# Optimization experiments

Hardware: AMD Instinct MI355X
Metric: run time of the kernel (lower is better)

The kernel has to match this reference:

```python
import jax, jax.numpy as jnp
import numpy as np

B, S, D, H, F, M, DC = 2, 1024, 1024, 16, 4096, 2048, 256
HD = D // H

def rmsnorm(x, w, eps=1e-6):
    return x * jax.lax.rsqrt(jnp.mean(x * x, axis=-1, keepdims=True) + eps) * w

def setup_inputs() -> dict:
    key = jax.random.key(0)
    ks = jax.random.split(key, 16)
    def w(i, shape):
        return jax.random.normal(ks[i], shape, jnp.float32) * (1.0 / np.sqrt(shape[0]))
    # real RoPE tables
    inv = 1.0 / (10000.0 ** (jnp.arange(0, HD, 2, dtype=jnp.float32) / HD))
    freqs = jnp.outer(jnp.arange(S, dtype=jnp.float32), inv)
    emb = jnp.concatenate([freqs, freqs], axis=-1)  # [S, HD]
    return {
        "hidden_states": jax.random.normal(ks[0], (B, S, D), jnp.float32),
        "mem_keys": jnp.zeros((B, M, DC), jnp.float32),
        "mem_values": jnp.zeros((B, M, D), jnp.float32),
        "cos": jnp.cos(emb), "sin": jnp.sin(emb),
        "norm1_w": jnp.ones((D,), jnp.float32),
        "norm2_w": jnp.ones((D,), jnp.float32),
        "norm_mem_w": jnp.ones((D,), jnp.float32),
        "Wq": w(1, (D, D)), "Wk": w(2, (D, D)), "Wv": w(3, (D, D)), "Wo": w(4, (D, D)),
        "W_content": w(5, (D, D)), "W_comp": w(6, (D, DC)), "W_strength": w(7, (D, 1)),
        "W_query": w(8, (D, DC)),
        "W_gate": w(9, (2 * D, D)), "W_proj": w(10, (D, D)),
        "W1": w(11, (D, F)), "W3": w(12, (D, F)), "W2": w(13, (F, D)),
        "position": 0,
    }

def reference(hidden_states, mem_keys, mem_values, cos, sin,
              norm1_w, norm2_w, norm_mem_w,
              Wq, Wk, Wv, Wo,
              W_content, W_comp, W_strength, W_query,
              W_gate, W_proj, W1, W3, W2, position):
    b, s, d = hidden_states.shape
    h = hidden_states
    # 1) causal self-attention with RoPE
    n = rmsnorm(h, norm1_w)
    def heads(x):
        return x.reshape(b, s, H, HD).transpose(0, 2, 1, 3)  # [b,h,s,hd]
    q, k, v = heads(n @ Wq), heads(n @ Wk), heads(n @ Wv)
    def rot(x):
        x1, x2 = jnp.split(x, 2, axis=-1)
        return jnp.concatenate([-x2, x1], axis=-1)
    c, si = cos[None, None], sin[None, None]
    q = q * c + rot(q) * si
    k = k * c + rot(k) * si
    scores = jnp.einsum('bhqd,bhkd->bhqk', q, k) / np.sqrt(HD)
    causal = jnp.tril(jnp.ones((s, s), bool))
    scores = jnp.where(causal, scores, jnp.float32(-1e30))
    attn = jax.nn.softmax(scores, axis=-1)
    attn_out = jnp.einsum('bhqk,bhkd->bhqd', attn, v).transpose(0, 2, 1, 3).reshape(b, s, d) @ Wo
    h = h + attn_out
    # 2) memory snapshot write: the original per-token python loop writes each token
    #    to consecutive circular-buffer slots; with M >= s the slots are unique, so
    #    the loop vectorizes into a single scatter.
    content = h @ W_content                     # [b,s,d]
    compressed = h @ W_comp                     # [b,s,DC]
    strength = jax.nn.sigmoid(h @ W_strength)   # [b,s,1]
    idx = (position + jnp.arange(s)) % mem_keys.shape[1]
    old_k = mem_keys[:, idx]
    old_v = mem_values[:, idx]
    new_keys = mem_keys.at[:, idx].set(strength * compressed + (1.0 - strength) * old_k)
    new_values = mem_values.at[:, idx].set(strength * content + (1.0 - strength) * old_v)
    # 3) memory retrieval (attention over slots)
    normed = rmsnorm(h, norm_mem_w)
    qm = normed @ W_query                       # [b,s,DC]
    mscores = jnp.einsum('bsd,bmd->bsm', qm, new_keys) / np.sqrt(DC)
    mattn = jax.nn.softmax(mscores, axis=-1)
    retrieved = jnp.einsum('bsm,bmd->bsd', mattn, new_values)
    # 4) gated memory integration
    gate = jax.nn.sigmoid(jnp.concatenate([h, retrieved], axis=-1) @ W_gate)
    h = h + gate * (retrieved @ W_proj)
    # 5) SwiGLU FFN
    n2 = rmsnorm(h, norm2_w)
    h = h + (jax.nn.silu(n2 @ W1) * (n2 @ W3)) @ W2
    return (h, new_keys, new_values)
```

## Files before the change

### kernel.cpp

```cpp
#include <hip/hip_runtime.h>
#include <hip/hip_bf16.h>
#include <math.h>

typedef __bf16 bf16;
typedef __attribute__((ext_vector_type(8))) __bf16 bf16x8;
typedef __attribute__((ext_vector_type(4))) __bf16 bf16x4;
typedef __attribute__((ext_vector_type(4))) float f32x4;

#define B_ 2
#define S_ 1024
#define D_ 1024
#define H_ 16
#define HD_ 64
#define F_ 4096
#define M_ 2048
#define DC_ 256
#define NTOK (B_*S_)

__device__ __forceinline__ void gload16(const void* g, void* l) {
    __builtin_amdgcn_global_load_lds(
        (__attribute__((address_space(1))) void*)(void*)(g),
        (__attribute__((address_space(3))) void*)(l), 16, 0, 0);
}

template<int N> __device__ __forceinline__ void wait_vm() {
    if constexpr (N == 0)      asm volatile("s_waitcnt vmcnt(0)" ::: "memory");
    else if constexpr (N == 2) asm volatile("s_waitcnt vmcnt(2)" ::: "memory");
    else if constexpr (N == 4) asm volatile("s_waitcnt vmcnt(4)" ::: "memory");
    else if constexpr (N == 6) asm volatile("s_waitcnt vmcnt(6)" ::: "memory");
    else                       asm volatile("s_waitcnt vmcnt(8)" ::: "memory");
}
__device__ __forceinline__ void wait_lgkm0() {
    asm volatile("s_waitcnt lgkmcnt(0)" ::: "memory");
}
__device__ __forceinline__ float sigm(float x) { return 1.f / (1.f + expf(-x)); }

template<int BM, int BN, bool OUTBF, int EPI>
__global__ __launch_bounds__(256) void mgemm(
    const bf16* __restrict__ A, const bf16* __restrict__ Bt,
    const float* __restrict__ resid, void* __restrict__ Cout,
    int K, int lda, int ldb, int ldc,
    long long sA, long long sB, long long sC,
    const void* __restrict__ aux1, const void* __restrict__ aux2)
{
    constexpr int WN   = (BM == 128) ? 2 : 4;
    constexpr int WCOL = BN / WN;
    constexpr int FN   = WCOL / 16;
    constexpr int LA = BM * 64, LB = BN * 64;
    constexpr int LPS = BM / 32 + BN / 32;
    __shared__ bf16 lds[2 * (LA + LB)];
    const int z = blockIdx.z;
    A  += (size_t)z * sA;
    Bt += (size_t)z * sB;
    const int gx = gridDim.x;
    const int nwg = gx * gridDim.y;
    const int flat = blockIdx.y * gx + blockIdx.x;
    const int q8 = nwg >> 3, r8 = nwg & 7;
    const int xcd = flat & 7, lid = flat >> 3;
    const int swz = (xcd < r8 ? xcd * (q8 + 1) : r8 * (q8 + 1) + (xcd - r8) * q8) + lid;
    const int band = swz / (8 * gx);
    const int rem  = swz % (8 * gx);
    const int row0 = (band * 8 + (rem & 7)) * BM;
    const int col0 = (rem >> 3) * BN;
    const int tid = threadIdx.x, wid = tid >> 6, lane = tid & 63;
    const int wr = wid / WN, wc = wid % WN;
    const int srow = lane >> 3;
    const int ssub = (lane & 7) ^ (srow & 7);

    f32x4 acc[4][FN];
    #pragma unroll
    for (int m = 0; m < 4; ++m)
        #pragma unroll
        for (int n = 0; n < FN; ++n) acc[m][n] = (f32x4){0.f, 0.f, 0.f, 0.f};

    auto STAGE = [&](int buf, int k0) {
        bf16* Ab = lds + buf * (LA + LB);
        bf16* Bb = Ab + LA;
        #pragma unroll
        for (int i = 0; i < BM / 32; ++i) {
            int c = wid * (BM / 32) + i;
            gload16(A + (size_t)(row0 + c * 8 + srow) * lda + k0 + ssub * 8, Ab + c * 512);
        }
        #pragma unroll
        for (int i = 0; i < BN / 32; ++i) {
            int c = wid * (BN / 32) + i;
            gload16(Bt + (size_t)(col0 + c * 8 + srow) * ldb + k0 + ssub * 8, Bb + c * 512);
        }
    };

    const int nt = K >> 6;
    STAGE(0, 0);
    if (nt > 1) STAGE(1, 64);
    for (int t = 0; t < nt; ++t) {
        if (t < nt - 1) wait_vm<LPS>();
        else            wait_vm<0>();
        __builtin_amdgcn_sched_barrier(0);
        __builtin_amdgcn_s_barrier();
        __builtin_amdgcn_sched_barrier(0);
        const bf16* Ab = lds + (t & 1) * (LA + LB);
        const bf16* Bb = Ab + LA;
        const int ar = wr * 64 + (lane & 15);
        const int br = wc * WCOL + (lane & 15);
        #pragma unroll
        for (int ksel = 0; ksel < 2; ++ksel) {
            const int ps = ((ksel << 2) + (lane >> 4)) ^ (lane & 7);
            bf16x8 af[4], bfr[FN];
            #pragma unroll
            for (int m = 0; m < 4; ++m)
                af[m] = *(const bf16x8*)(Ab + (ar + m * 16) * 64 + ps * 8);
            #pragma unroll
            for (int n = 0; n < FN; ++n)
                bfr[n] = *(const bf16x8*)(Bb + (br + n * 16) * 64 + ps * 8);
            #pragma unroll
            for (int m = 0; m < 4; ++m)
                #pragma unroll
                for (int n = 0; n < FN; ++n)
                    acc[m][n] = __builtin_amdgcn_mfma_f32_16x16x32_bf16(af[m], bfr[n], acc[m][n], 0, 0, 0);
        }
        wait_lgkm0();
        __builtin_amdgcn_sched_barrier(0);
        __builtin_amdgcn_s_barrier();
        __builtin_amdgcn_sched_barrier(0);
        if (t + 2 < nt) STAGE(t & 1, (t + 2) << 6);
    }
    const int crow = row0 + wr * 64 + ((lane >> 4) << 2);
    const int ccol = col0 + wc * WCOL + (lane & 15);
    #pragma unroll
    for (int m = 0; m < 4; ++m)
        #pragma unroll
        for (int n = 0; n < FN; ++n)
            #pragma unroll
            for (int r = 0; r < 4; ++r) {
                const int rr = crow + m * 16 + r, cc = ccol + n * 16;
                size_t idx = (size_t)rr * ldc + cc;
                float v = acc[m][n][r];
                if (EPI == 2) {
                    float g = sigm(((const float*)aux1)[idx]);
                    v = ((const float*)aux2)[idx] + g * v;
                    ((float*)Cout)[idx] = v;
                } else {
                    if (resid) v += resid[idx];
                    if (OUTBF) ((bf16*)Cout)[(size_t)z * sC + idx] = (bf16)v;
                    else       ((float*)Cout)[(size_t)z * sC + idx] = v;
                    if (EPI == 1)
                        ((bf16*)aux1)[(size_t)rr * 2048 + cc] = (bf16)v;
                }
            }
}

__global__ __launch_bounds__(256) void mgemm13(
    const bf16* __restrict__ A, const bf16* __restrict__ B1t, const bf16* __restrict__ B3t,
    bf16* __restrict__ Cout, int K, int lda, int ldb, int ldc)
{
    constexpr int LA = 128 * 64, LB = 64 * 64;
    __shared__ bf16 lds[2 * (LA + 2 * LB)];
    const int gx = gridDim.x;
    const int nwg = gx * gridDim.y;
    const int flat = blockIdx.y * gx + blockIdx.x;
    const int q8 = nwg >> 3, r8 = nwg & 7;
    const int xcd = flat & 7, lid = flat >> 3;
    const int swz = (xcd < r8 ? xcd * (q8 + 1) : r8 * (q8 + 1) + (xcd - r8) * q8) + lid;
    const int band = swz / (8 * gx);
    const int rem  = swz % (8 * gx);
    const int row0 = (band * 8 + (rem & 7)) * 128;
    const int col0 = (rem >> 3) * 64;
    const int tid = threadIdx.x, wid = tid >> 6, lane = tid & 63;
    const int wr = wid >> 1, wc = wid & 1;
    const int srow = lane >> 3;
    const int ssub = (lane & 7) ^ (srow & 7);

    f32x4 acc1[4][2], acc3[4][2];
    #pragma unroll
    for (int m = 0; m < 4; ++m)
        #pragma unroll
        for (int n = 0; n < 2; ++n) {
            acc1[m][n] = (f32x4){0.f, 0.f, 0.f, 0.f};
            acc3[m][n] = (f32x4){0.f, 0.f, 0.f, 0.f};
        }

    auto STAGE = [&](int buf, int k0) {
        bf16* Ab = lds + buf * (LA + 2 * LB);
        bf16* B1b = Ab + LA;
        bf16* B3b = B1b + LB;
        #pragma unroll
        for (int i = 0; i < 4; ++i) {
            int c = wid * 4 + i;
            gload16(A + (size_t)(row0 + c * 8 + srow) * lda + k0 + ssub * 8, Ab + c * 512);
        }
        #pragma unroll
        for (int i = 0; i < 2; ++i) {
            int c = wid * 2 + i;
            gload16(B1t + (size_t)(col0 + c * 8 + srow) * ldb + k0 + ssub * 8, B1b + c * 512);
            gload16(B3t + (size_t)(col0 + c * 8 + srow) * ldb + k0 + ssub * 8, B3b + c * 512);
        }
    };

    const int nt = K >> 6;
    STAGE(0, 0);
    if (nt > 1) STAGE(1, 64);
    for (int t = 0; t < nt; ++t) {
        if (t < nt - 1) wait_vm<8>();
        else            wait_vm<0>();
        __builtin_amdgcn_sched_barrier(0);
        __builtin_amdgcn_s_barrier();
        __builtin_amdgcn_sched_barrier(0);
        const bf16* Ab = lds + (t & 1) * (LA + 2 * LB);
        const bf16* B1b = Ab + LA;
        const bf16* B3b = B1b + LB;
        const int ar = wr * 64 + (lane & 15);
        const int br = wc * 32 + (lane & 15);
        #pragma unroll
        for (int ksel = 0; ksel < 2; ++ksel) {
            const int ps = ((ksel << 2) + (lane >> 4)) ^ (lane & 7);
            bf16x8 af[4], b1f[2], b3f[2];
            #pragma unroll
            for (int m = 0; m < 4; ++m)
                af[m] = *(const bf16x8*)(Ab + (ar + m * 16) * 64 + ps * 8);
            #pragma unroll
            for (int n = 0; n < 2; ++n) {
                b1f[n] = *(const bf16x8*)(B1b + (br + n * 16) * 64 + ps * 8);
                b3f[n] = *(const bf16x8*)(B3b + (br + n * 16) * 64 + ps * 8);
            }
            #pragma unroll
            for (int m = 0; m < 4; ++m)
                #pragma unroll
                for (int n = 0; n < 2; ++n) {
                    acc1[m][n] = __builtin_amdgcn_mfma_f32_16x16x32_bf16(af[m], b1f[n], acc1[m][n], 0, 0, 0);
                    acc3[m][n] = __builtin_amdgcn_mfma_f32_16x16x32_bf16(af[m], b3f[n], acc3[m][n], 0, 0, 0);
                }
        }
        wait_lgkm0();
        __builtin_amdgcn_sched_barrier(0);
        __builtin_amdgcn_s_barrier();
        __builtin_amdgcn_sched_barrier(0);
        if (t + 2 < nt) STAGE(t & 1, (t + 2) << 6);
    }
    const int crow = row0 + wr * 64 + ((lane >> 4) << 2);
    const int ccol = col0 + wc * 32 + (lane & 15);
    #pragma unroll
    for (int m = 0; m < 4; ++m)
        #pragma unroll
        for (int n = 0; n < 2; ++n)
            #pragma unroll
            for (int r = 0; r < 4; ++r) {
                float x = acc1[m][n][r];
                float v = (x * sigm(x)) * acc3[m][n][r];
                Cout[(size_t)(crow + m * 16 + r) * ldc + ccol + n * 16] = (bf16)v;
            }
}

__global__ __launch_bounds__(256) void flash_attn(
    const bf16* __restrict__ qkv, const bf16* __restrict__ vt,
    bf16* __restrict__ o)
{
    __shared__ bf16 qlds[64 * 64];
    __shared__ bf16 klds[2][64 * 64];
    __shared__ bf16 vlds[2][64 * 64];
    __shared__ bf16 plds[4][16 * 64];
    const int qt = blockIdx.x, hh = blockIdx.y, b = blockIdx.z;
    const int qb0 = qt * 64;
    const int tid = threadIdx.x, wid = tid >> 6, lane = tid & 63;
    const bf16* qg = qkv + (size_t)b * S_ * 3072 + hh * 64;
    const bf16* kg = qg + 1024;
    const bf16* vg = vt + (size_t)(b * H_ + hh) * 64 * 1024;
    const int srow = lane >> 3;
    const int ssub = (lane & 7) ^ (srow & 7);

    #pragma unroll
    for (int i = 0; i < 2; ++i) {
        int c = wid * 2 + i;
        gload16(qg + (size_t)(qb0 + c * 8 + srow) * 3072 + ssub * 8, qlds + c * 512);
    }
    auto STAGE = [&](int buf, int kb) {
        #pragma unroll
        for (int i = 0; i < 2; ++i) {
            int c = wid * 2 + i;
            gload16(kg + (size_t)(kb + c * 8 + srow) * 3072 + ssub * 8, klds[buf] + c * 512);
            gload16(vg + (size_t)(c * 8 + srow) * 1024 + kb + ssub * 8, vlds[buf] + c * 512);
        }
    };

    const int nt = qt + 1;
    STAGE(0, 0);
    if (nt > 1) STAGE(1, 64);

    f32x4 oacc[4];
    #pragma unroll
    for (int n = 0; n < 4; ++n) oacc[n] = (f32x4){0.f, 0.f, 0.f, 0.f};
    float mrow[4] = {-1e30f, -1e30f, -1e30f, -1e30f};
    float lrow[4] = {0.f, 0.f, 0.f, 0.f};
    bf16x8 qf[2];
    bf16* pw = plds[wid];
    const int qlr = (lane >> 4) * 4;

    for (int t = 0; t < nt; ++t) {
        if (t < nt - 1) wait_vm<4>();
        else            wait_vm<0>();
        __builtin_amdgcn_sched_barrier(0);
        __builtin_amdgcn_s_barrier();
        __builtin_amdgcn_sched_barrier(0);
        if (t == 0) {
            const int ar = wid * 16 + (lane & 15);
            #pragma unroll
            for (int ksel = 0; ksel < 2; ++ksel) {
                const int ps = ((ksel << 2) + (lane >> 4)) ^ (lane & 7);
                qf[ksel] = *(const bf16x8*)(qlds + ar * 64 + ps * 8);
            }
        }
        const bf16* Kb = klds[t & 1];
        const bf16* Vb = vlds[t & 1];
        f32x4 sacc[4];
        #pragma unroll
        for (int n = 0; n < 4; ++n) sacc[n] = (f32x4){0.f, 0.f, 0.f, 0.f};
        #pragma unroll
        for (int ksel = 0; ksel < 2; ++ksel) {
            const int ps = ((ksel << 2) + (lane >> 4)) ^ (lane & 7);
            #pragma unroll
            for (int n = 0; n < 4; ++n) {
                bf16x8 kf = *(const bf16x8*)(Kb + (n * 16 + (lane & 15)) * 64 + ps * 8);
                sacc[n] = __builtin_amdgcn_mfma_f32_16x16x32_bf16(qf[ksel], kf, sacc[n], 0, 0, 0);
            }
        }
        if (t == nt - 1) {
            const int qrow = qb0 + wid * 16 + qlr;
            const int kcol = t * 64 + (lane & 15);
            #pragma unroll
            for (int n = 0; n < 4; ++n)
                #pragma unroll
                for (int r = 0; r < 4; ++r)
                    if (kcol + n * 16 > qrow + r) sacc[n][r] = -1e30f;
        }
        #pragma unroll
        for (int r = 0; r < 4; ++r) {
            float mx = fmaxf(fmaxf(sacc[0][r], sacc[1][r]), fmaxf(sacc[2][r], sacc[3][r]));
            #pragma unroll
            for (int off = 8; off > 0; off >>= 1) mx = fmaxf(mx, __shfl_xor(mx, off));
            float mnew = fmaxf(mrow[r], mx);
            float scale = __expf(mrow[r] - mnew);
            float rs = 0.f;
            #pragma unroll
            for (int n = 0; n < 4; ++n) {
                float p = __expf(sacc[n][r] - mnew);
                sacc[n][r] = p;
                rs += p;
            }
            #pragma unroll
            for (int off = 8; off > 0; off >>= 1) rs += __shfl_xor(rs, off);
            lrow[r] = lrow[r] * scale + rs;
            mrow[r] = mnew;
            #pragma unroll
            for (int n = 0; n < 4; ++n) oacc[n][r] *= scale;
        }
        #pragma unroll
        for (int n = 0; n < 4; ++n)
            #pragma unroll
            for (int r = 0; r < 4; ++r) {
                const int qr = qlr + r;
                const int k = n * 16 + (lane & 15);
                const int su = (k >> 3) ^ (qr & 7);
                pw[qr * 64 + su * 8 + (k & 7)] = (bf16)sacc[n][r];
            }
        #pragma unroll
        for (int ksel = 0; ksel < 2; ++ksel) {
            const int ps = ((ksel << 2) + (lane >> 4)) ^ (lane & 7);
            bf16x8 pa = *(const bf16x8*)(pw + (lane & 15) * 64 + ps * 8);
            #pragma unroll
            for (int n = 0; n < 4; ++n) {
                bf16x8 vf = *(const bf16x8*)(Vb + (n * 16 + (lane & 15)) * 64 + ps * 8);
                oacc[n] = __builtin_amdgcn_mfma_f32_16x16x32_bf16(pa, vf, oacc[n], 0, 0, 0);
            }
        }
        wait_lgkm0();
        __builtin_amdgcn_sched_barrier(0);
        __builtin_amdgcn_s_barrier();
        __builtin_amdgcn_sched_barrier(0);
        if (t + 2 < nt) STAGE(t & 1, (t + 2) * 64);
    }
    float inv[4];
    #pragma unroll
    for (int r = 0; r < 4; ++r) inv[r] = 1.f / lrow[r];
    #pragma unroll
    for (int n = 0; n < 4; ++n)
        #pragma unroll
        for (int r = 0; r < 4; ++r) {
            const int q = qb0 + wid * 16 + qlr + r;
            const int d = n * 16 + (lane & 15);
            o[(size_t)(b * S_ + q) * 1024 + hh * 64 + d] = (bf16)(oacc[n][r] * inv[r]);
        }
}

template<typename TI>
__global__ __launch_bounds__(256) void tcast(
    const TI* __restrict__ in, bf16* __restrict__ out,
    int lin, int lout, long long sin, long long sout)
{
    __shared__ float t[32][33];
    in  += (size_t)blockIdx.z * sin;
    out += (size_t)blockIdx.z * sout;
    const int c0 = blockIdx.x * 32, r0 = blockIdx.y * 32;
    const int tx = threadIdx.x & 31, ty = threadIdx.x >> 5;
    #pragma unroll
    for (int j = 0; j < 4; ++j)
        t[ty + j * 8][tx] = (float)in[(size_t)(r0 + ty + j * 8) * lin + c0 + tx];
    __syncthreads();
    #pragma unroll
    for (int j = 0; j < 4; ++j)
        out[(size_t)(c0 + ty + j * 8) * lout + r0 + tx] = (bf16)t[tx][ty + j * 8];
}

struct TC6 { const float* in[6]; bf16* out[6]; };
__global__ __launch_bounds__(256) void tcast_b(TC6 p, int lin, int lout)
{
    __shared__ float t[32][33];
    const float* in = p.in[blockIdx.z];
    bf16* out = p.out[blockIdx.z];
    const int c0 = blockIdx.x * 32, r0 = blockIdx.y * 32;
    const int tx = threadIdx.x & 31, ty = threadIdx.x >> 5;
    #pragma unroll
    for (int j = 0; j < 4; ++j)
        t[ty + j * 8][tx] = in[(size_t)(r0 + ty + j * 8) * lin + c0 + tx];
    __syncthreads();
    #pragma unroll
    for (int j = 0; j < 4; ++j)
        out[(size_t)(c0 + ty + j * 8) * lout + r0 + tx] = (bf16)t[tx][ty + j * 8];
}

__global__ __launch_bounds__(256) void rmsnorm_bf(
    const float* __restrict__ x, const float* __restrict__ w, bf16* __restrict__ out)
{
    __shared__ float red[4];
    const int row = blockIdx.x, tid = threadIdx.x;
    const float* xr = x + (size_t)row * D_;
    f32x4 v = *(const f32x4*)(xr + tid * 4);
    float ss = v.x * v.x + v.y * v.y + v.z * v.z + v.w * v.w;
    #pragma unroll
    for (int off = 32; off > 0; off >>= 1) ss += __shfl_xor(ss, off);
    if ((tid & 63) == 0) red[tid >> 6] = ss;
    __syncthreads();
    float scn = rsqrtf((red[0] + red[1] + red[2] + red[3]) * (1.f / D_) + 1e-6f);
    f32x4 wv = *(const f32x4*)(w + tid * 4);
    bf16x4 o;
    o[0] = (bf16)(v.x * scn * wv.x); o[1] = (bf16)(v.y * scn * wv.y);
    o[2] = (bf16)(v.z * scn * wv.z); o[3] = (bf16)(v.w * scn * wv.w);
    *(bf16x4*)(out + (size_t)row * D_ + tid * 4) = o;
}

__global__ void rope_kernel(bf16* __restrict__ qkv,
                            const float* __restrict__ cosp, const float* __restrict__ sinp)
{
    int idx = blockIdx.x * 256 + threadIdx.x;
    int p = idx & 31, hh = (idx >> 5) & 15, s = (idx >> 9) & 1023, b = idx >> 19;
    size_t base = ((size_t)(b * S_ + s)) * 3072 + hh * 64;
    float c1 = cosp[s * 64 + p],      s1 = sinp[s * 64 + p];
    float c2 = cosp[s * 64 + p + 32], s2 = sinp[s * 64 + p + 32];
    float q1 = (float)qkv[base + p], q2 = (float)qkv[base + p + 32];
    qkv[base + p]      = (bf16)((q1 * c1 - q2 * s1) * 0.125f);
    qkv[base + p + 32] = (bf16)((q2 * c2 + q1 * s2) * 0.125f);
    size_t kb = base + 1024;
    float k1 = (float)qkv[kb + p], k2 = (float)qkv[kb + p + 32];
    qkv[kb + p]      = (bf16)(k1 * c1 - k2 * s1);
    qkv[kb + p + 32] = (bf16)(k2 * c2 + k1 * s2);
}

__global__ __launch_bounds__(256) void mem_softmax(
    const float* __restrict__ ms, bf16* __restrict__ out)
{
    __shared__ float red[4];
    const int row = blockIdx.x, tid = threadIdx.x;
    const float* r = ms + (size_t)row * 2048;
    f32x4 a = *(const f32x4*)(r + tid * 8);
    f32x4 b = *(const f32x4*)(r + tid * 8 + 4);
    float xs[8] = {a.x, a.y, a.z, a.w, b.x, b.y, b.z, b.w};
    float mx = -1e30f;
    #pragma unroll
    for (int i = 0; i < 8; ++i) mx = fmaxf(mx, xs[i]);
    #pragma unroll
    for (int off = 32; off > 0; off >>= 1) mx = fmaxf(mx, __shfl_xor(mx, off));
    if ((tid & 63) == 0) red[tid >> 6] = mx;
    __syncthreads();
    mx = fmaxf(fmaxf(red[0], red[1]), fmaxf(red[2], red[3]));
    __syncthreads();
    float sum = 0.f;
    #pragma unroll
    for (int i = 0; i < 8; ++i) { xs[i] = __expf((xs[i] - mx) * 0.0625f); sum += xs[i]; }
    #pragma unroll
    for (int off = 32; off > 0; off >>= 1) sum += __shfl_xor(sum, off);
    if ((tid & 63) == 0) red[tid >> 6] = sum;
    __syncthreads();
    float inv = 1.f / (red[0] + red[1] + red[2] + red[3]);
    bf16x8 o;
    #pragma unroll
    for (int i = 0; i < 8; ++i) o[i] = (bf16)(xs[i] * inv);
    *(bf16x8*)(out + (size_t)row * 2048 + tid * 8) = o;
}

__global__ void strength_kernel(const float* __restrict__ h, const float* __restrict__ ws,
                                float* __restrict__ st)
{
    const int row = blockIdx.x, lane = threadIdx.x;
    const float* hr = h + (size_t)row * D_;
    float s = 0.f;
    #pragma unroll
    for (int it = 0; it < 4; ++it) {
        f32x4 hv = *(const f32x4*)(hr + it * 256 + lane * 4);
        f32x4 wv = *(const f32x4*)(ws + it * 256 + lane * 4);
        s += hv.x * wv.x + hv.y * wv.y + hv.z * wv.z + hv.w * wv.w;
    }
    #pragma unroll
    for (int off = 32; off > 0; off >>= 1) s += __shfl_xor(s, off);
    if (lane == 0) st[row] = sigm(s);
}

__global__ void mem_upd_k(const float* __restrict__ ctcp, const float* __restrict__ st,
                          const float* __restrict__ memk, const int* __restrict__ pos,
                          float* __restrict__ outk, bf16* __restrict__ okbf)
{
    int idx = blockIdx.x * 256 + threadIdx.x;
    int c = (idx & 63) * 4;
    int row = (idx >> 6) & (M_ - 1);
    int b = idx >> 17;
    int s = (row - pos[0]) % M_; if (s < 0) s += M_;
    size_t mi = ((size_t)b * M_ + row) * DC_ + c;
    f32x4 o = *(const f32x4*)(memk + mi);
    if (s < S_) {
        float t = st[b * S_ + s];
        f32x4 cv = *(const f32x4*)(ctcp + ((size_t)b * S_ + s) * 1280 + 1024 + c);
        o.x = t * cv.x + (1.f - t) * o.x; o.y = t * cv.y + (1.f - t) * o.y;
        o.z = t * cv.z + (1.f - t) * o.z; o.w = t * cv.w + (1.f - t) * o.w;
    }
    *(f32x4*)(outk + mi) = o;
    bf16x4 ob = {(bf16)o.x, (bf16)o.y, (bf16)o.z, (bf16)o.w};
    *(bf16x4*)(okbf + mi) = ob;
}

__global__ void mem_upd_v(const float* __restrict__ ctcp, const float* __restrict__ st,
                          const float* __restrict__ memv, const int* __restrict__ pos,
                          float* __restrict__ outv)
{
    int idx = blockIdx.x * 256 + threadIdx.x;
    int c = (idx & 255) * 4;
    int row = (idx >> 8) & (M_ - 1);
    int b = idx >> 19;
    int s = (row - pos[0]) % M_; if (s < 0) s += M_;
    size_t mi = ((size_t)b * M_ + row) * D_ + c;
    f32x4 o = *(const f32x4*)(memv + mi);
    if (s < S_) {
        float t = st[b * S_ + s];
        f32x4 cv = *(const f32x4*)(ctcp + ((size_t)b * S_ + s) * 1280 + c);
        o.x = t * cv.x + (1.f - t) * o.x; o.y = t * cv.y + (1.f - t) * o.y;
        o.z = t * cv.z + (1.f - t) * o.z; o.w = t * cv.w + (1.f - t) * o.w;
    }
    *(f32x4*)(outv + mi) = o;
}

extern "C" void kernel_launch(void* const* d_in, const int* in_sizes, int n_in,
                              void* d_out, int out_size, void* d_ws, size_t ws_size,
                              hipStream_t stream)
{
    const float* h0   = (const float*)d_in[0];
    const float* memk = (const float*)d_in[1];
    const float* memv = (const float*)d_in[2];
    const float* cosp = (const float*)d_in[3];
    const float* sinp = (const float*)d_in[4];
    const float* n1w  = (const float*)d_in[5];
    const float* n2w  = (const float*)d_in[6];
    const float* nmw  = (const float*)d_in[7];
    const float* Wq   = (const float*)d_in[8];
    const float* Wk   = (const float*)d_in[9];
    const float* Wv   = (const float*)d_in[10];
    const float* Wo   = (const float*)d_in[11];
    const float* Wct  = (const float*)d_in[12];
    const float* Wcp  = (const float*)d_in[13];
    const float* Wst  = (const float*)d_in[14];
    const float* Wqr  = (const float*)d_in[15];
    const float* Wg   = (const float*)d_in[16];
    const float* Wpj  = (const float*)d_in[17];
    const float* W1   = (const float*)d_in[18];
    const float* W3   = (const float*)d_in[19];
    const float* W2   = (const float*)d_in[20];
    const int*   pos  = (const int*)d_in[21];

    float* out_h = (float*)d_out;
    float* out_k = out_h + (size_t)NTOK * D_;
    float* out_v = out_k + (size_t)B_ * M_ * DC_;

    char* W = (char*)d_ws;
    const size_t MB = 1u << 20;
    bf16*  qkvb = (bf16*)(W);
    bf16*  vtb  = (bf16*)(W + 12 * MB);
    bf16*  nbf  = (bf16*)(W + 16 * MB);
    bf16*  abf  = (bf16*)(W + 20 * MB);
    float* h1b  = (float*)(W + 24 * MB);
    bf16*  catbf= (bf16*)(W + 32 * MB);
    float* ctcp = (float*)(W + 40 * MB);
    float* stb  = (float*)(W + 51 * MB);
    float* msb  = (float*)(W + 52 * MB);
    bf16*  matt = (bf16*)(W + 68 * MB);
    bf16*  nvt  = (bf16*)(W + 76 * MB);
    bf16*  a1bf = (bf16*)(W);
    bf16*  okbf = (bf16*)(W + 84 * MB);
    bf16*  qmbf = (bf16*)(W + 86 * MB);
    float* aob  = (float*)(W + 88 * MB);
    float* h2b  = (float*)(W + 96 * MB);
    bf16*  WqkvT= (bf16*)(W + 104 * MB);
    bf16*  WoT  = (bf16*)(W + 110 * MB);
    bf16*  WctcpT=(bf16*)(W + 112 * MB);
    bf16*  WqrT = (bf16*)(W + 115 * MB);
    bf16*  WgT  = (bf16*)(W + 116 * MB);
    bf16*  WpjT = (bf16*)(W + 120 * MB);
    bf16*  W13T = (bf16*)(W + 122 * MB);
    bf16*  W2T  = (bf16*)(W + 138 * MB);

    {
        TC6 pa;
        pa.in[0] = Wq;  pa.out[0] = WqkvT;
        pa.in[1] = Wk;  pa.out[1] = WqkvT + 1024 * 1024;
        pa.in[2] = Wv;  pa.out[2] = WqkvT + 2048 * 1024;
        pa.in[3] = Wo;  pa.out[3] = WoT;
        pa.in[4] = Wct; pa.out[4] = WctcpT;
        pa.in[5] = Wpj; pa.out[5] = WpjT;
        tcast_b<<<dim3(32, 32, 6), 256, 0, stream>>>(pa, 1024, 1024);
        TC6 pb;
        pb.in[0] = Wcp; pb.out[0] = WctcpT + 1024 * 1024;
        pb.in[1] = Wqr; pb.out[1] = WqrT;
        pb.in[2] = Wcp; pb.out[2] = WctcpT + 1024 * 1024;
        pb.in[3] = Wcp; pb.out[3] = WctcpT + 1024 * 1024;
        pb.in[4] = Wcp; pb.out[4] = WctcpT + 1024 * 1024;
        pb.in[5] = Wcp; pb.out[5] = WctcpT + 1024 * 1024;
        tcast_b<<<dim3(8, 32, 2), 256, 0, stream>>>(pb, 256, 1024);
        TC6 pc;
        pc.in[0] = W1; pc.out[0] = W13T;
        pc.in[1] = W3; pc.out[1] = W13T + 4096 * 1024;
        pc.in[2] = W1; pc.out[2] = W13T;
        pc.in[3] = W1; pc.out[3] = W13T;
        pc.in[4] = W1; pc.out[4] = W13T;
        pc.in[5] = W1; pc.out[5] = W13T;
        tcast_b<<<dim3(128, 32, 2), 256, 0, stream>>>(pc, 4096, 1024);
    }
    tcast<float><<<dim3(32, 64, 1), 256, 0, stream>>>(Wg, WgT, 1024, 2048, 0, 0);
    tcast<float><<<dim3(32, 128, 1), 256, 0, stream>>>(W2, W2T, 1024, 4096, 0, 0);

    rmsnorm_bf<<<NTOK, 256, 0, stream>>>(h0, n1w, nbf);
    mgemm<64, 128, true, 0><<<dim3(24, 32, 1), 256, 0, stream>>>(
        nbf, WqkvT, nullptr, qkvb, 1024, 1024, 1024, 3072, 0, 0, 0, nullptr, nullptr);
    rope_kernel<<<(B_ * S_ * H_ * 32) / 256, 256, 0, stream>>>(qkvb, cosp, sinp);
    for (int b = 0; b < B_; ++b)
        tcast<bf16><<<dim3(2, 32, 16), 256, 0, stream>>>(
            qkvb + (size_t)b * S_ * 3072 + 2048, vtb + (size_t)b * 16 * 65536,
            3072, 1024, 64, 65536);

    flash_attn<<<dim3(S_ / 64, H_, B_), 256, 0, stream>>>(qkvb, vtb, abf);

    mgemm<64, 64, false, 1><<<dim3(16, 32, 1), 256, 0, stream>>>(
        abf, WoT, h0, h1b, 1024, 1024, 1024, 1024, 0, 0, 0, catbf, nullptr);
    strength_kernel<<<NTOK, 64, 0, stream>>>(h1b, Wst, stb);

    mgemm<64, 64, false, 0><<<dim3(20, 32, 1), 256, 0, stream>>>(
        catbf, WctcpT, nullptr, ctcp, 1024, 2048, 1024, 1280, 0, 0, 0, nullptr, nullptr);
    mem_upd_k<<<(B_ * M_ * DC_) / 1024, 256, 0, stream>>>(ctcp, stb, memk, pos, out_k, okbf);
    mem_upd_v<<<(B_ * M_ * D_) / 1024, 256, 0, stream>>>(ctcp, stb, memv, pos, out_v);

    rmsnorm_bf<<<NTOK, 256, 0, stream>>>(h1b, nmw, nbf);
    mgemm<64, 64, true, 0><<<dim3(4, 32, 1), 256, 0, stream>>>(
        nbf, WqrT, nullptr, qmbf, 1024, 1024, 1024, 256, 0, 0, 0, nullptr, nullptr);
    mgemm<64, 128, false, 0><<<dim3(16, 16, 2), 256, 0, stream>>>(
        qmbf, okbf, nullptr, msb, 256, 256, 256, 2048,
        (long long)S_ * 256, (long long)M_ * 256, (long long)S_ * 2048, nullptr, nullptr);
    mem_softmax<<<NTOK, 256, 0, stream>>>(msb, matt);
    tcast<float><<<dim3(32, 64, 2), 256, 0, stream>>>(
        out_v, nvt, 1024, 2048, (long long)M_ * 1024, (long long)1024 * 2048);
    mgemm<64, 128, true, 0><<<dim3(8, 16, 2), 256, 0, stream>>>(
        matt, nvt, nullptr, catbf + 1024, 2048, 2048, 2048, 2048,
        (long long)S_ * 2048, (long long)1024 * 2048, (long long)S_ * 2048, nullptr, nullptr);

    mgemm<64, 64, false, 0><<<dim3(16, 32, 1), 256, 0, stream>>>(
        catbf, WgT, nullptr, aob, 2048, 2048, 2048, 1024, 0, 0, 0, nullptr, nullptr);
    mgemm<64, 64, false, 2><<<dim3(16, 32, 1), 256, 0, stream>>>(
        catbf + 1024, WpjT, nullptr, h2b, 1024, 2048, 1024, 1024, 0, 0, 0, aob, h1b);

    rmsnorm_bf<<<NTOK, 256, 0, stream>>>(h2b, n2w, nbf);
    mgemm13<<<dim3(64, 16, 1), 256, 0, stream>>>(
        nbf, W13T, W13T + 4096 * 1024, a1bf, 1024, 1024, 1024, 4096);
    mgemm<64, 64, false, 0><<<dim3(16, 32, 1), 256, 0, stream>>>(
        a1bf, W2T, h2b, out_h, 4096, 4096, 4096, 1024, 0, 0, 0, nullptr, nullptr);
}
```

Baseline: 296.8 us.

## Fuse RoPE with V transpose, merge small kernels, store intermediates as bf16

```diff
diff --git a/kernel.cpp b/kernel.cpp
--- a/kernel.cpp
+++ b/kernel.cpp
@@ -135,7 +135,7 @@
                 size_t idx = (size_t)rr * ldc + cc;
                 float v = acc[m][n][r];
                 if (EPI == 2) {
-                    float g = sigm(((const float*)aux1)[idx]);
+                    float g = sigm((float)((const bf16*)aux1)[idx]);
                     v = ((const float*)aux2)[idx] + g * v;
                     ((float*)Cout)[idx] = v;
                 } else {
@@ -445,35 +445,104 @@
     *(bf16x4*)(out + (size_t)row * D_ + tid * 4) = o;
 }
 
-__global__ void rope_kernel(bf16* __restrict__ qkv,
-                            const float* __restrict__ cosp, const float* __restrict__ sinp)
-{
-    int idx = blockIdx.x * 256 + threadIdx.x;
-    int p = idx & 31, hh = (idx >> 5) & 15, s = (idx >> 9) & 1023, b = idx >> 19;
-    size_t base = ((size_t)(b * S_ + s)) * 3072 + hh * 64;
-    float c1 = cosp[s * 64 + p],      s1 = sinp[s * 64 + p];
-    float c2 = cosp[s * 64 + p + 32], s2 = sinp[s * 64 + p + 32];
-    float q1 = (float)qkv[base + p], q2 = (float)qkv[base + p + 32];
-    qkv[base + p]      = (bf16)((q1 * c1 - q2 * s1) * 0.125f);
-    qkv[base + p + 32] = (bf16)((q2 * c2 + q1 * s2) * 0.125f);
-    size_t kb = base + 1024;
-    float k1 = (float)qkv[kb + p], k2 = (float)qkv[kb + p + 32];
-    qkv[kb + p]      = (bf16)(k1 * c1 - k2 * s1);
-    qkv[kb + p + 32] = (bf16)(k2 * c2 + k1 * s2);
+__global__ __launch_bounds__(256) void h1_post(
+    const float* __restrict__ h1, const float* __restrict__ nmw,
+    const float* __restrict__ wst, bf16* __restrict__ nbf, float* __restrict__ stb)
+{
+    __shared__ float red[4], red2[4];
+    const int row = blockIdx.x, tid = threadIdx.x;
+    const float* xr = h1 + (size_t)row * D_;
+    f32x4 v = *(const f32x4*)(xr + tid * 4);
+    f32x4 wv = *(const f32x4*)(wst + tid * 4);
+    float ss = v.x * v.x + v.y * v.y + v.z * v.z + v.w * v.w;
+    float dt = v.x * wv.x + v.y * wv.y + v.z * wv.z + v.w * wv.w;
+    #pragma unroll
+    for (int off = 32; off > 0; off >>= 1) {
+        ss += __shfl_xor(ss, off);
+        dt += __shfl_xor(dt, off);
+    }
+    if ((tid & 63) == 0) { red[tid >> 6] = ss; red2[tid >> 6] = dt; }
+    __syncthreads();
+    float scn = rsqrtf((red[0] + red[1] + red[2] + red[3]) * (1.f / D_) + 1e-6f);
+    f32x4 nw = *(const f32x4*)(nmw + tid * 4);
+    bf16x4 o;
+    o[0] = (bf16)(v.x * scn * nw.x); o[1] = (bf16)(v.y * scn * nw.y);
+    o[2] = (bf16)(v.z * scn * nw.z); o[3] = (bf16)(v.w * scn * nw.w);
+    *(bf16x4*)(nbf + (size_t)row * D_ + tid * 4) = o;
+    if (tid == 0) stb[row] = sigm(red2[0] + red2[1] + red2[2] + red2[3]);
+}
+
+__global__ __launch_bounds__(256) void rope_vt(
+    bf16* __restrict__ qkv, const float* __restrict__ cosp,
+    const float* __restrict__ sinp, bf16* __restrict__ vt)
+{
+    __shared__ bf16 vl[64][72];
+    const int st = blockIdx.x, hh = blockIdx.y, b = blockIdx.z;
+    const int tid = threadIdx.x;
+    const int r = tid >> 2;
+    const int p0 = (tid & 3) * 8;
+    const int s = st * 64 + r;
+    bf16* base = qkv + ((size_t)(b * S_ + s)) * 3072 + hh * 64;
+    {
+        f32x4 c1a = *(const f32x4*)(cosp + s * 64 + p0);
+        f32x4 c1b = *(const f32x4*)(cosp + s * 64 + p0 + 4);
+        f32x4 s1a = *(const f32x4*)(sinp + s * 64 + p0);
+        f32x4 s1b = *(const f32x4*)(sinp + s * 64 + p0 + 4);
+        f32x4 c2a = *(const f32x4*)(cosp + s * 64 + p0 + 32);
+        f32x4 c2b = *(const f32x4*)(cosp + s * 64 + p0 + 36);
+        f32x4 s2a = *(const f32x4*)(sinp + s * 64 + p0 + 32);
+        f32x4 s2b = *(const f32x4*)(sinp + s * 64 + p0 + 36);
+        float c1[8] = {c1a.x,c1a.y,c1a.z,c1a.w,c1b.x,c1b.y,c1b.z,c1b.w};
+        float s1[8] = {s1a.x,s1a.y,s1a.z,s1a.w,s1b.x,s1b.y,s1b.z,s1b.w};
+        float c2[8] = {c2a.x,c2a.y,c2a.z,c2a.w,c2b.x,c2b.y,c2b.z,c2b.w};
+        float s2[8] = {s2a.x,s2a.y,s2a.z,s2a.w,s2b.x,s2b.y,s2b.z,s2b.w};
+        #pragma unroll
+        for (int which = 0; which < 2; ++which) {
+            bf16* ptr = base + which * 1024;
+            bf16x8 x1 = *(const bf16x8*)(ptr + p0);
+            bf16x8 x2 = *(const bf16x8*)(ptr + p0 + 32);
+            bf16x8 o1, o2;
+            float qs = which ? 1.f : 0.125f;
+            #pragma unroll
+            for (int j = 0; j < 8; ++j) {
+                float a = (float)x1[j], bb = (float)x2[j];
+                o1[j] = (bf16)((a * c1[j] - bb * s1[j]) * qs);
+                o2[j] = (bf16)((bb * c2[j] + a * s2[j]) * qs);
+            }
+            *(bf16x8*)(ptr + p0) = o1;
+            *(bf16x8*)(ptr + p0 + 32) = o2;
+        }
+    }
+    {
+        const int d0 = (tid & 3) * 16;
+        bf16x8 v0 = *(const bf16x8*)(base + 2048 + d0);
+        bf16x8 v1 = *(const bf16x8*)(base + 2048 + d0 + 8);
+        #pragma unroll
+        for (int j = 0; j < 8; ++j) { vl[r][d0 + j] = v0[j]; vl[r][d0 + 8 + j] = v1[j]; }
+    }
+    __syncthreads();
+    {
+        const int d = tid >> 2;
+        const int sq = (tid & 3) * 16;
+        bf16x8 o0, o1;
+        #pragma unroll
+        for (int j = 0; j < 8; ++j) { o0[j] = vl[sq + j][d]; o1[j] = vl[sq + 8 + j][d]; }
+        bf16* dst = vt + (size_t)(b * H_ + hh) * 65536 + (size_t)d * 1024 + st * 64 + sq;
+        *(bf16x8*)(dst) = o0;
+        *(bf16x8*)(dst + 8) = o1;
+    }
 }
 
 __global__ __launch_bounds__(256) void mem_softmax(
-    const float* __restrict__ ms, bf16* __restrict__ out)
+    const bf16* __restrict__ ms, bf16* __restrict__ out)
 {
     __shared__ float red[4];
     const int row = blockIdx.x, tid = threadIdx.x;
-    const float* r = ms + (size_t)row * 2048;
-    f32x4 a = *(const f32x4*)(r + tid * 8);
-    f32x4 b = *(const f32x4*)(r + tid * 8 + 4);
-    float xs[8] = {a.x, a.y, a.z, a.w, b.x, b.y, b.z, b.w};
+    bf16x8 iv = *(const bf16x8*)(ms + (size_t)row * 2048 + tid * 8);
+    float xs[8];
     float mx = -1e30f;
     #pragma unroll
-    for (int i = 0; i < 8; ++i) mx = fmaxf(mx, xs[i]);
+    for (int i = 0; i < 8; ++i) { xs[i] = (float)iv[i]; mx = fmaxf(mx, xs[i]); }
     #pragma unroll
     for (int off = 32; off > 0; off >>= 1) mx = fmaxf(mx, __shfl_xor(mx, off));
     if ((tid & 63) == 0) red[tid >> 6] = mx;
@@ -494,63 +563,46 @@
     *(bf16x8*)(out + (size_t)row * 2048 + tid * 8) = o;
 }
 
-__global__ void strength_kernel(const float* __restrict__ h, const float* __restrict__ ws,
-                                float* __restrict__ st)
-{
-    const int row = blockIdx.x, lane = threadIdx.x;
-    const float* hr = h + (size_t)row * D_;
-    float s = 0.f;
-    #pragma unroll
-    for (int it = 0; it < 4; ++it) {
-        f32x4 hv = *(const f32x4*)(hr + it * 256 + lane * 4);
-        f32x4 wv = *(const f32x4*)(ws + it * 256 + lane * 4);
-        s += hv.x * wv.x + hv.y * wv.y + hv.z * wv.z + hv.w * wv.w;
-    }
-    #pragma unroll
-    for (int off = 32; off > 0; off >>= 1) s += __shfl_xor(s, off);
-    if (lane == 0) st[row] = sigm(s);
-}
-
-__global__ void mem_upd_k(const float* __restrict__ ctcp, const float* __restrict__ st,
-                          const float* __restrict__ memk, const int* __restrict__ pos,
-                          float* __restrict__ outk, bf16* __restrict__ okbf)
+__global__ void mem_upd(const float* __restrict__ ctcp, const float* __restrict__ st,
+                        const float* __restrict__ memk, const float* __restrict__ memv,
+                        const int* __restrict__ pos,
+                        float* __restrict__ outk, float* __restrict__ outv,
+                        bf16* __restrict__ okbf)
 {
     int idx = blockIdx.x * 256 + threadIdx.x;
-    int c = (idx & 63) * 4;
-    int row = (idx >> 6) & (M_ - 1);
-    int b = idx >> 17;
-    int s = (row - pos[0]) % M_; if (s < 0) s += M_;
-    size_t mi = ((size_t)b * M_ + row) * DC_ + c;
-    f32x4 o = *(const f32x4*)(memk + mi);
-    if (s < S_) {
-        float t = st[b * S_ + s];
-        f32x4 cv = *(const f32x4*)(ctcp + ((size_t)b * S_ + s) * 1280 + 1024 + c);
-        o.x = t * cv.x + (1.f - t) * o.x; o.y = t * cv.y + (1.f - t) * o.y;
-        o.z = t * cv.z + (1.f - t) * o.z; o.w = t * cv.w + (1.f - t) * o.w;
-    }
-    *(f32x4*)(outk + mi) = o;
-    bf16x4 ob = {(bf16)o.x, (bf16)o.y, (bf16)o.z, (bf16)o.w};
-    *(bf16x4*)(okbf + mi) = ob;
-}
-
-__global__ void mem_upd_v(const float* __restrict__ ctcp, const float* __restrict__ st,
-                          const float* __restrict__ memv, const int* __restrict__ pos,
-                          float* __restrict__ outv)
-{
-    int idx = blockIdx.x * 256 + threadIdx.x;
-    int c = (idx & 255) * 4;
-    int row = (idx >> 8) & (M_ - 1);
-    int b = idx >> 19;
-    int s = (row - pos[0]) % M_; if (s < 0) s += M_;
-    size_t mi = ((size_t)b * M_ + row) * D_ + c;
-    f32x4 o = *(const f32x4*)(memv + mi);
-    if (s < S_) {
-        float t = st[b * S_ + s];
-        f32x4 cv = *(const f32x4*)(ctcp + ((size_t)b * S_ + s) * 1280 + c);
-        o.x = t * cv.x + (1.f - t) * o.x; o.y = t * cv.y + (1.f - t) * o.y;
-        o.z = t * cv.z + (1.f - t) * o.z; o.w = t * cv.w + (1.f - t) * o.w;
-    }
-    *(f32x4*)(outv + mi) = o;
+    const int NV = B_ * M_ * D_ / 4;
+    if (idx < NV) {
+        int c = (idx & 255) * 4;
+        int row = (idx >> 8) & (M_ - 1);
+        int b = idx >> 19;
+        int s = (row - pos[0]) % M_; if (s < 0) s += M_;
+        size_t mi = ((size_t)b * M_ + row) * D_ + c;
+        f32x4 o = *(const f32x4*)(memv + mi);
+        if (s < S_) {
+            float t = st[b * S_ + s];
+            f32x4 cv = *(const f32x4*)(ctcp + ((size_t)b * S_ + s) * 1280 + c);
+            o.x = t * cv.x + (1.f - t) * o.x; o.y = t * cv.y + (1.f - t) * o.y;
+            o.z = t * cv.z + (1.f - t) * o.z; o.w = t * cv.w + (1.f - t) * o.w;
+        }
+        *(f32x4*)(outv + mi) = o;
+    } else {
+        idx -= NV;
+        int c = (idx & 63) * 4;
+        int row = (idx >> 6) & (M_ - 1);
+        int b = idx >> 17;
+        int s = (row - pos[0]) % M_; if (s < 0) s += M_;
+        size_t mi = ((size_t)b * M_ + row) * DC_ + c;
+        f32x4 o = *(const f32x4*)(memk + mi);
+        if (s < S_) {
+            float t = st[b * S_ + s];
+            f32x4 cv = *(const f32x4*)(ctcp + ((size_t)b * S_ + s) * 1280 + 1024 + c);
+            o.x = t * cv.x + (1.f - t) * o.x; o.y = t * cv.y + (1.f - t) * o.y;
+            o.z = t * cv.z + (1.f - t) * o.z; o.w = t * cv.w + (1.f - t) * o.w;
+        }
+        *(f32x4*)(outk + mi) = o;
+        bf16x4 ob = {(bf16)o.x, (bf16)o.y, (bf16)o.z, (bf16)o.w};
+        *(bf16x4*)(okbf + mi) = ob;
+    }
 }
 
 extern "C" void kernel_launch(void* const* d_in, const int* in_sizes, int n_in,
@@ -594,13 +646,13 @@
     bf16*  catbf= (bf16*)(W + 32 * MB);
     float* ctcp = (float*)(W + 40 * MB);
     float* stb  = (float*)(W + 51 * MB);
-    float* msb  = (float*)(W + 52 * MB);
+    bf16*  msbf = (bf16*)(W + 52 * MB);
     bf16*  matt = (bf16*)(W + 68 * MB);
     bf16*  nvt  = (bf16*)(W + 76 * MB);
     bf16*  a1bf = (bf16*)(W);
     bf16*  okbf = (bf16*)(W + 84 * MB);
     bf16*  qmbf = (bf16*)(W + 86 * MB);
-    float* aob  = (float*)(W + 88 * MB);
+    bf16*  aobf = (bf16*)(W + 88 * MB);
     float* h2b  = (float*)(W + 96 * MB);
     bf16*  WqkvT= (bf16*)(W + 104 * MB);
     bf16*  WoT  = (bf16*)(W + 110 * MB);
@@ -643,40 +695,35 @@
     rmsnorm_bf<<<NTOK, 256, 0, stream>>>(h0, n1w, nbf);
     mgemm<64, 128, true, 0><<<dim3(24, 32, 1), 256, 0, stream>>>(
         nbf, WqkvT, nullptr, qkvb, 1024, 1024, 1024, 3072, 0, 0, 0, nullptr, nullptr);
-    rope_kernel<<<(B_ * S_ * H_ * 32) / 256, 256, 0, stream>>>(qkvb, cosp, sinp);
-    for (int b = 0; b < B_; ++b)
-        tcast<bf16><<<dim3(2, 32, 16), 256, 0, stream>>>(
-            qkvb + (size_t)b * S_ * 3072 + 2048, vtb + (size_t)b * 16 * 65536,
-            3072, 1024, 64, 65536);
+    rope_vt<<<dim3(S_ / 64, H_, B_), 256, 0, stream>>>(qkvb, cosp, sinp, vtb);
 
     flash_attn<<<dim3(S_ / 64, H_, B_), 256, 0, stream>>>(qkvb, vtb, abf);
 
     mgemm<64, 64, false, 1><<<dim3(16, 32, 1), 256, 0, stream>>>(
         abf, WoT, h0, h1b, 1024, 1024, 1024, 1024, 0, 0, 0, catbf, nullptr);
-    strength_kernel<<<NTOK, 64, 0, stream>>>(h1b, Wst, stb);
+    h1_post<<<NTOK, 256, 0, stream>>>(h1b, nmw, Wst, nbf, stb);
 
     mgemm<64, 64, false, 0><<<dim3(20, 32, 1), 256, 0, stream>>>(
         catbf, WctcpT, nullptr, ctcp, 1024, 2048, 1024, 1280, 0, 0, 0, nullptr, nullptr);
-    mem_upd_k<<<(B_ * M_ * DC_) / 1024, 256, 0, stream>>>(ctcp, stb, memk, pos, out_k, okbf);
-    mem_upd_v<<<(B_ * M_ * D_) / 1024, 256, 0, stream>>>(ctcp, stb, memv, pos, out_v);
-
-    rmsnorm_bf<<<NTOK, 256, 0, stream>>>(h1b, nmw, nbf);
+    mem_upd<<<(B_ * M_ * D_ / 4 + B_ * M_ * DC_ / 4) / 256, 256, 0, stream>>>(
+        ctcp, stb, memk, memv, pos, out_k, out_v, okbf);
+
     mgemm<64, 64, true, 0><<<dim3(4, 32, 1), 256, 0, stream>>>(
         nbf, WqrT, nullptr, qmbf, 1024, 1024, 1024, 256, 0, 0, 0, nullptr, nullptr);
-    mgemm<64, 128, false, 0><<<dim3(16, 16, 2), 256, 0, stream>>>(
-        qmbf, okbf, nullptr, msb, 256, 256, 256, 2048,
+    mgemm<64, 128, true, 0><<<dim3(16, 16, 2), 256, 0, stream>>>(
+        qmbf, okbf, nullptr, msbf, 256, 256, 256, 2048,
         (long long)S_ * 256, (long long)M_ * 256, (long long)S_ * 2048, nullptr, nullptr);
-    mem_softmax<<<NTOK, 256, 0, stream>>>(msb, matt);
+    mem_softmax<<<NTOK, 256, 0, stream>>>(msbf, matt);
     tcast<float><<<dim3(32, 64, 2), 256, 0, stream>>>(
         out_v, nvt, 1024, 2048, (long long)M_ * 1024, (long long)1024 * 2048);
     mgemm<64, 128, true, 0><<<dim3(8, 16, 2), 256, 0, stream>>>(
         matt, nvt, nullptr, catbf + 1024, 2048, 2048, 2048, 2048,
         (long long)S_ * 2048, (long long)1024 * 2048, (long long)S_ * 2048, nullptr, nullptr);
 
-    mgemm<64, 64, false, 0><<<dim3(16, 32, 1), 256, 0, stream>>>(
-        catbf, WgT, nullptr, aob, 2048, 2048, 2048, 1024, 0, 0, 0, nullptr, nullptr);
+    mgemm<64, 64, true, 0><<<dim3(16, 32, 1), 256, 0, stream>>>(
+        catbf, WgT, nullptr, aobf, 2048, 2048, 2048, 1024, 0, 0, 0, nullptr, nullptr);
     mgemm<64, 64, false, 2><<<dim3(16, 32, 1), 256, 0, stream>>>(
-        catbf + 1024, WpjT, nullptr, h2b, 1024, 2048, 1024, 1024, 0, 0, 0, aob, h1b);
+        catbf + 1024, WpjT, nullptr, h2b, 1024, 2048, 1024, 1024, 0, 0, 0, aobf, h1b);
 
     rmsnorm_bf<<<NTOK, 256, 0, stream>>>(h2b, n2w, nbf);
     mgemm13<<<dim3(64, 16, 1), 256, 0, stream>>>(
```

New measurement: 284.3 us. -4.2%, faster.
